# Performance work log

Measured on AMD Instinct MI355X. Metric: run time of the kernel, lower is better.

Reference implementation:

```python
import math
import jax, jax.numpy as jnp
import numpy as np

N_NODES = 50000
N_EDGES = 600000
IN_CH = 64      # in_channels == out_channels (residual requires it)
HEADS = 2
C = 64          # per-head dim == out_channels
HC = HEADS * C  # 128
EDGE_DIM = 32


def setup_inputs() -> dict:
    key = jax.random.key(0)
    ks = jax.random.split(key, 12)
    s = 0.05
    return {
        "x": jax.random.normal(ks[0], (N_NODES, IN_CH), jnp.float32),
        "edge_index": jax.random.randint(ks[1], (2, N_EDGES), 0, N_NODES, dtype=jnp.int64),
        "edge_attr": jax.random.normal(ks[2], (N_EDGES, EDGE_DIM), jnp.float32),
        "Wq": s * jax.random.normal(ks[3], (IN_CH, HC), jnp.float32),
        "bq": jnp.zeros((HC,), jnp.float32),
        "Wk": s * jax.random.normal(ks[4], (IN_CH, HC), jnp.float32),
        "bk": jnp.zeros((HC,), jnp.float32),
        "Wv": s * jax.random.normal(ks[5], (IN_CH, HC), jnp.float32),
        "bv": jnp.zeros((HC,), jnp.float32),
        "We": s * jax.random.normal(ks[6], (EDGE_DIM, HC), jnp.float32),
        "Wp": s * jax.random.normal(ks[7], (HC, IN_CH), jnp.float32),
        "bp": jnp.zeros((IN_CH,), jnp.float32),
        "ln1_g": jnp.ones((IN_CH,), jnp.float32),
        "ln1_b": jnp.zeros((IN_CH,), jnp.float32),
        "ln2_g": jnp.ones((IN_CH,), jnp.float32),
        "ln2_b": jnp.zeros((IN_CH,), jnp.float32),
        "W1": s * jax.random.normal(ks[8], (IN_CH, IN_CH), jnp.float32),
        "b1": jnp.zeros((IN_CH,), jnp.float32),
        "W2": s * jax.random.normal(ks[9], (IN_CH, IN_CH), jnp.float32),
        "b2": jnp.zeros((IN_CH,), jnp.float32),
    }


def _layernorm(x, g, b, eps=1e-5):
    m = jnp.mean(x, axis=-1, keepdims=True)
    v = jnp.mean(jnp.square(x - m), axis=-1, keepdims=True)
    return (x - m) / jnp.sqrt(v + eps) * g + b


def reference(x, edge_index, edge_attr, Wq, bq, Wk, bk, Wv, bv, We, Wp, bp,
              ln1_g, ln1_b, ln2_g, ln2_b, W1, b1, W2, b2):
    n = x.shape[0]
    residual = x
    h = _layernorm(x, ln1_g, ln1_b)
    q = (h @ Wq + bq).reshape(n, HEADS, C)
    k = (h @ Wk + bk).reshape(n, HEADS, C)
    v = (h @ Wv + bv).reshape(n, HEADS, C)

    src, tgt = edge_index[0], edge_index[1]
    e = (edge_attr @ We).reshape(-1, HEADS, C)   # (E,H,C)
    qi = q[tgt]                                  # (E,H,C) gather by target
    kj = k[src] + e
    vj = v[src] + e

    alpha = jnp.sum(qi * kj, axis=-1) / math.sqrt(C)            # (E,H)
    amax = jax.ops.segment_max(alpha, tgt, num_segments=n)      # (N,H)
    ex = jnp.exp(alpha - amax[tgt])
    den = jax.ops.segment_sum(ex, tgt, num_segments=n)          # (N,H)
    a = ex / (den[tgt] + 1e-8)                                  # (E,H)

    agg = jax.ops.segment_sum(a[:, :, None] * vj, tgt, num_segments=n)  # (N,H,C)
    out = agg.reshape(n, HC) @ Wp + bp
    out = out + residual                        # in_channels == out_channels

    res2 = out
    o = _layernorm(out, ln2_g, ln2_b)
    o = jax.nn.gelu(o @ W1 + b1, approximate=False) @ W2 + b2
    return o + res2
```

## Files before the change

### kernel.cpp

```cpp
#include <hip/hip_runtime.h>
#include <math.h>
#include <stdint.h>


typedef float f32x4 __attribute__((ext_vector_type(4)));
typedef __bf16 bf16x8 __attribute__((ext_vector_type(8)));
typedef unsigned int u32x4 __attribute__((ext_vector_type(4)));

#define WPM_S 200
#define W1_OFF 12800
#define W2_OFF 18432
#define W_TOT 24064
#define H_S 72
#define WC_S 72
#define WC_TOT (448 * 72)

__device__ __forceinline__ unsigned pack_bf16(float2 v) {
    unsigned a = __builtin_bit_cast(unsigned, v.x);
    unsigned b = __builtin_bit_cast(unsigned, v.y);
    a = (a + 0x7FFFu + ((a >> 16) & 1u)) >> 16;
    b = (b + 0x7FFFu + ((b >> 16) & 1u)) >> 16;
    return a | (b << 16);
}
__device__ __forceinline__ float2 unpack_bf16(unsigned p) {
    float x = __builtin_bit_cast(float, p << 16);
    float y = __builtin_bit_cast(float, p & 0xFFFF0000u);
    return make_float2(x, y);
}
__device__ __forceinline__ unsigned short bf16r(float x) {
    unsigned u = __builtin_bit_cast(unsigned, x);
    return (unsigned short)((u + 0x7FFFu + ((u >> 16) & 1u)) >> 16);
}

__device__ __forceinline__ f32x4 mfma16(bf16x8 a, bf16x8 b, f32x4 c) {
    return __builtin_amdgcn_mfma_f32_16x16x32_bf16(a, b, c, 0, 0, 0);
}
__device__ __forceinline__ bf16x8 frag_ld(const unsigned short* p) {
    return __builtin_bit_cast(bf16x8, *(const u32x4*)p);
}

__global__ void k_pre(const float* __restrict__ Wq, const float* __restrict__ Wk,
                      const float* __restrict__ Wv, const float* __restrict__ We,
                      const float* __restrict__ Wp, const float* __restrict__ W1,
                      const float* __restrict__ W2, const float* __restrict__ bq,
                      const float* __restrict__ bk, const float* __restrict__ bv,
                      unsigned short* __restrict__ wsW,
                      unsigned short* __restrict__ wcat, float* __restrict__ bcat,
                      int* __restrict__ deg, int n) {
    int idx = blockIdx.x * 256 + threadIdx.x;
    for (int i = idx; i < n; i += gridDim.x * 256) deg[i] = 0;
    if (idx < 8192) {
        int o = idx >> 7, k = idx & 127;
        wsW[o * WPM_S + k] = bf16r(Wp[((k & 1) * 64 + (k >> 1)) * 64 + o]);
        int cin = idx >> 7, j = idx & 127;
        wcat[j * WC_S + cin] = bf16r(Wq[cin * 128 + j]);
        wcat[(128 + j) * WC_S + cin] = bf16r(Wk[cin * 128 + j]);
        wcat[(256 + j) * WC_S + cin] = bf16r(Wv[cin * 128 + j]);
    }
    if (idx < 4096) {
        int o = idx >> 6, k = idx & 63;
        wsW[W1_OFF + o * 88 + k] = bf16r(W1[k * 64 + o]);
        wsW[W2_OFF + o * 88 + k] = bf16r(W2[k * 64 + o]);
        int o2 = idx & 63, dh = idx >> 6, d = dh >> 1, h = dh & 1;
        float s = 0.f;
        for (int c = 0; c < 64; ++c)
            s += We[d * 128 + h * 64 + c] * Wp[(h * 64 + c) * 64 + o2];
        wsW[o2 * WPM_S + 128 + dh] = bf16r(s);
        int cin2 = idx & 63, dh2 = idx >> 6, d2 = dh2 >> 1, h2 = dh2 & 1;
        float s2 = 0.f;
        for (int c = 0; c < 64; ++c)
            s2 += Wq[cin2 * 128 + h2 * 64 + c] * We[d2 * 128 + h2 * 64 + c];
        wcat[(384 + dh2) * WC_S + cin2] = bf16r(s2);
    }
    if (idx < 384)
        bcat[idx] = idx < 128 ? bq[idx] : idx < 256 ? bk[idx - 128] : bv[idx - 256];
    if (idx < 64) {
        int d = idx >> 1, h = idx & 1;
        float s = 0.f;
        for (int c = 0; c < 64; ++c)
            s += bq[h * 64 + c] * We[d * 128 + h * 64 + c];
        bcat[384 + idx] = s;
    }
}

__global__ __launch_bounds__(256) void k_bucket(
    const int* __restrict__ ei, int* __restrict__ deg,
    int* __restrict__ bucket_e, unsigned short* __restrict__ bucket_s,
    int E, int n) {
    int e = blockIdx.x * 256 + threadIdx.x;
    if (e >= E) return;
    int src = ei[e], tgt = ei[E + e];
    src = min(max(src, 0), n - 1);
    tgt = min(max(tgt, 0), n - 1);
    int slot = atomicAdd(&deg[tgt], 1);
    if (slot < 64) {
        bucket_e[(size_t)tgt * 64 + slot] = e;
        bucket_s[(size_t)tgt * 64 + slot] = (unsigned short)src;
    }
}

__global__ __launch_bounds__(256) void k_qkv(
    const float* __restrict__ x, const unsigned short* __restrict__ wcat,
    const float* __restrict__ bcat,
    const float* __restrict__ g1, const float* __restrict__ b1,
    unsigned* __restrict__ qx, unsigned* __restrict__ kbf,
    unsigned* __restrict__ vbf, int n) {
    __shared__ __align__(16) unsigned short sW[WC_TOT];
    int tid = threadIdx.x;
    for (int i = tid; i < WC_TOT / 8; i += 256)
        ((u32x4*)sW)[i] = ((const u32x4*)wcat)[i];
    __syncthreads();

    int wave = tid >> 6, lane = tid & 63;
    int cl = lane & 15, kg = lane >> 4;
    int node0 = blockIdx.x * 64 + wave * 16;
    if (node0 >= n) return;
    int arow = min(node0 + cl, n - 1);

    const float4* xp = (const float4*)(x + (size_t)arow * 64);
    float4 xv[4] = {xp[kg * 2], xp[kg * 2 + 1], xp[8 + kg * 2], xp[9 + kg * 2]};
    float s1 = 0.f, s2 = 0.f;
#pragma unroll
    for (int i = 0; i < 4; ++i) {
        s1 += (xv[i].x + xv[i].y) + (xv[i].z + xv[i].w);
        s2 += xv[i].x * xv[i].x + xv[i].y * xv[i].y
            + xv[i].z * xv[i].z + xv[i].w * xv[i].w;
    }
    s1 += __shfl_xor(s1, 16); s2 += __shfl_xor(s2, 16);
    s1 += __shfl_xor(s1, 32); s2 += __shfl_xor(s2, 32);
    float mean = s1 * 0.015625f;
    float var  = s2 * 0.015625f - mean * mean;
    float rstd = rsqrtf(var + 1e-5f);
    const float4* gp = (const float4*)g1;
    const float4* bp1 = (const float4*)b1;
    float4 gv[4] = {gp[kg * 2], gp[kg * 2 + 1], gp[8 + kg * 2], gp[9 + kg * 2]};
    float4 bv4[4] = {bp1[kg * 2], bp1[kg * 2 + 1], bp1[8 + kg * 2], bp1[9 + kg * 2]};
    unsigned fr[8];
#pragma unroll
    for (int i = 0; i < 4; ++i) {
        float h0 = (xv[i].x - mean) * rstd * gv[i].x + bv4[i].x;
        float h1 = (xv[i].y - mean) * rstd * gv[i].y + bv4[i].y;
        float h2 = (xv[i].z - mean) * rstd * gv[i].z + bv4[i].z;
        float h3 = (xv[i].w - mean) * rstd * gv[i].w + bv4[i].w;
        fr[i * 2]     = pack_bf16(make_float2(h0, h1));
        fr[i * 2 + 1] = pack_bf16(make_float2(h2, h3));
    }
    bf16x8 A0 = __builtin_bit_cast(bf16x8, (u32x4){fr[0], fr[1], fr[2], fr[3]});
    bf16x8 A1 = __builtin_bit_cast(bf16x8, (u32x4){fr[4], fr[5], fr[6], fr[7]});

#pragma unroll
    for (int tq = 0; tq < 4; ++tq) {
        int c = tq * 16 + cl;
        f32x4 aq0 = {bcat[c], bcat[c], bcat[c], bcat[c]};
        float b_;
        b_ = bcat[64 + c];  f32x4 aq1 = {b_, b_, b_, b_};
        b_ = bcat[128 + c]; f32x4 ak0 = {b_, b_, b_, b_};
        b_ = bcat[192 + c]; f32x4 ak1 = {b_, b_, b_, b_};
        b_ = bcat[256 + c]; f32x4 av0 = {b_, b_, b_, b_};
        b_ = bcat[320 + c]; f32x4 av1 = {b_, b_, b_, b_};
        b_ = bcat[384 + c]; f32x4 aw  = {b_, b_, b_, b_};
#pragma unroll
        for (int s = 0; s < 2; ++s) {
            bf16x8 A = s ? A1 : A0;
            int ko = s * 32 + kg * 8;
            aq0 = mfma16(A, frag_ld(sW + (size_t)(c) * WC_S + ko), aq0);
            aq1 = mfma16(A, frag_ld(sW + (size_t)(64 + c) * WC_S + ko), aq1);
            ak0 = mfma16(A, frag_ld(sW + (size_t)(128 + c) * WC_S + ko), ak0);
            ak1 = mfma16(A, frag_ld(sW + (size_t)(192 + c) * WC_S + ko), ak1);
            av0 = mfma16(A, frag_ld(sW + (size_t)(256 + c) * WC_S + ko), av0);
            av1 = mfma16(A, frag_ld(sW + (size_t)(320 + c) * WC_S + ko), av1);
            aw  = mfma16(A, frag_ld(sW + (size_t)(384 + c) * WC_S + ko), aw);
        }
#pragma unroll
        for (int j = 0; j < 4; ++j) {
            int node = node0 + kg * 4 + j;
            if (node < n) {
                qx[(size_t)node * 128 + c] = pack_bf16(make_float2(aq0[j], aq1[j]));
                kbf[(size_t)node * 64 + c] = pack_bf16(make_float2(ak0[j], ak1[j]));
                vbf[(size_t)node * 64 + c] = pack_bf16(make_float2(av0[j], av1[j]));
                ((float*)qx)[(size_t)node * 128 + 64 + c] = aw[j];
            }
        }
    }
}

__global__ __launch_bounds__(256) void k_attn(
    const unsigned* __restrict__ qx, const unsigned* __restrict__ kbf,
    const unsigned* __restrict__ vbf, const float* __restrict__ edge_attr,
    const int* __restrict__ deg, const int* __restrict__ bucket_e,
    const unsigned short* __restrict__ bucket_s,
    unsigned* __restrict__ aggs, int n, int E) {
    int wave = threadIdx.x >> 6, lane = threadIdx.x & 63;
    int node = blockIdx.x * 4 + wave;
    if (node >= n) return;
    int sub = lane >> 4, l = lane & 15;

    uint4 qq = ((const uint4*)qx)[(size_t)node * 32 + l];
    float4 w4 = ((const float4*)qx)[(size_t)node * 32 + 16 + l];
    float2 q0 = unpack_bf16(qq.x), q1 = unpack_bf16(qq.y),
           q2 = unpack_bf16(qq.z), q3 = unpack_bf16(qq.w);

    int dcount = min(deg[node], 64);
    int eid_l = 0, src_l = 0;
    if (lane < dcount) {
        eid_l = min(max(bucket_e[(size_t)node * 64 + lane], 0), E - 1);
        src_l = min((int)bucket_s[(size_t)node * 64 + lane], n - 1);
    }

    const uint4* kb4 = (const uint4*)kbf;
    const uint4* vb4 = (const uint4*)vbf;
    const float2* ea2 = (const float2*)edge_attr;

    float accA[4] = {0.f, 0.f, 0.f, 0.f}, accB[4] = {0.f, 0.f, 0.f, 0.f};
    float aS0 = 0.f, aS1 = 0.f, bS0 = 0.f, bS1 = 0.f;
    float den0 = 0.f, den1 = 0.f;

    uint4 kk, vv; float2 a2;
    {
        int jj = sub & 63;
        int ej = __shfl(eid_l, jj), sj = __shfl(src_l, jj);
        kk = kb4[(size_t)sj * 16 + l];
        vv = vb4[(size_t)sj * 16 + l];
        a2 = ea2[(size_t)ej * 16 + l];
    }
    for (int i = 0; i < dcount; i += 4) {
        uint4 kc = kk, vc = vv; float2 ac = a2;
        bool valid = (i + sub) < dcount;
        int inx = i + 4;
        if (inx < dcount) {
            int jj = (inx + sub) & 63;
            int ej = __shfl(eid_l, jj), sj = __shfl(src_l, jj);
            kk = kb4[(size_t)sj * 16 + l];
            vv = vb4[(size_t)sj * 16 + l];
            a2 = ea2[(size_t)ej * 16 + l];
        }
        float2 k0 = unpack_bf16(kc.x), k1 = unpack_bf16(kc.y),
               k2 = unpack_bf16(kc.z), k3 = unpack_bf16(kc.w);
        float r0 = q0.x * k0.x + q1.x * k1.x + q2.x * k2.x + q3.x * k3.x
                 + w4.x * ac.x + w4.z * ac.y;
        float r1 = q0.y * k0.y + q1.y * k1.y + q2.y * k2.y + q3.y * k3.y
                 + w4.y * ac.x + w4.w * ac.y;
#pragma unroll
        for (int m = 1; m < 16; m <<= 1) {
            r0 += __shfl_xor(r0, m);
            r1 += __shfl_xor(r1, m);
        }
        float ex0 = valid ? __expf(r0 * 0.125f) : 0.f;
        float ex1 = valid ? __expf(r1 * 0.125f) : 0.f;
        float2 v0 = unpack_bf16(vc.x), v1 = unpack_bf16(vc.y),
               v2 = unpack_bf16(vc.z), v3 = unpack_bf16(vc.w);
        accA[0] += ex0 * v0.x; accB[0] += ex1 * v0.y;
        accA[1] += ex0 * v1.x; accB[1] += ex1 * v1.y;
        accA[2] += ex0 * v2.x; accB[2] += ex1 * v2.y;
        accA[3] += ex0 * v3.x; accB[3] += ex1 * v3.y;
        aS0 += ex0 * ac.x; aS1 += ex1 * ac.x;
        bS0 += ex0 * ac.y; bS1 += ex1 * ac.y;
        den0 += ex0; den1 += ex1;
    }

#pragma unroll
    for (int m = 16; m < 64; m <<= 1) {
#pragma unroll
        for (int j = 0; j < 4; ++j) {
            accA[j] += __shfl_xor(accA[j], m);
            accB[j] += __shfl_xor(accB[j], m);
        }
        aS0 += __shfl_xor(aS0, m); aS1 += __shfl_xor(aS1, m);
        bS0 += __shfl_xor(bS0, m); bS1 += __shfl_xor(bS1, m);
        den0 += __shfl_xor(den0, m); den1 += __shfl_xor(den1, m);
    }

    float r0 = 1.0f / (den0 + 1e-8f);
    float r1 = 1.0f / (den1 + 1e-8f);

    float va = sub == 0 ? accA[0] : sub == 1 ? accA[1] : sub == 2 ? accA[2] : accA[3];
    float vb = sub == 0 ? accB[0] : sub == 1 ? accB[1] : sub == 2 ? accB[2] : accB[3];
    aggs[(size_t)node * 96 + 4 * l + sub] =
        pack_bf16(make_float2(va * r0, vb * r1));

    if (sub == 0) {
        unsigned s0 = pack_bf16(make_float2(aS0 * r0, aS1 * r1));
        unsigned s1 = pack_bf16(make_float2(bS0 * r0, bS1 * r1));
        *(uint2*)&aggs[(size_t)node * 96 + 64 + 2 * l] = make_uint2(s0, s1);
    }
}

__global__ __launch_bounds__(256) void k_post(
    const unsigned short* __restrict__ aggsb,
    const unsigned short* __restrict__ wsW,
    const float* __restrict__ bp, const float* __restrict__ x,
    const float* __restrict__ g2, const float* __restrict__ b2,
    const float* __restrict__ b1f, const float* __restrict__ b2f,
    float* __restrict__ out, int n) {
    __shared__ __align__(16) unsigned short sW[W_TOT];
    __shared__ __align__(16) unsigned short hb[4][2][16 * H_S];
    int tid = threadIdx.x;
    for (int i = tid; i < W_TOT / 8; i += 256)
        ((u32x4*)sW)[i] = ((const u32x4*)wsW)[i];
    __syncthreads();

    int wave = tid >> 6, lane = tid & 63;
    int cl = lane & 15, kg = lane >> 4;
    unsigned short* h2 = hb[wave][0];
    unsigned short* h3 = hb[wave][1];

    float bp_c[4], g2_c[4], b2_c[4], b1_c[4], bf2_c[4];
#pragma unroll
    for (int t = 0; t < 4; ++t) {
        int c = t * 16 + cl;
        bp_c[t] = bp[c];
        g2_c[t] = g2[c];
        b2_c[t] = b2[c];
        b1_c[t] = b1f[c];
        bf2_c[t] = b2f[c];
    }

    int wid = blockIdx.x * 4 + wave;
    int nbatch = (n + 15) >> 4;
    int nwaves = gridDim.x * 4;
    for (int bt = wid; bt < nbatch; bt += nwaves) {
        int node0 = bt * 16;

        f32x4 acc1[4];
#pragma unroll
        for (int t = 0; t < 4; ++t) acc1[t] = (f32x4){0.f, 0.f, 0.f, 0.f};
        int arow = min(node0 + cl, n - 1);
#pragma unroll
        for (int s = 0; s < 6; ++s) {
            bf16x8 af = frag_ld(aggsb + (size_t)arow * 192 + s * 32 + kg * 8);
#pragma unroll
            for (int t = 0; t < 4; ++t) {
                bf16x8 bf = frag_ld(sW + (t * 16 + cl) * WPM_S + s * 32 + kg * 8);
                acc1[t] = mfma16(af, bf, acc1[t]);
            }
        }
#pragma unroll
        for (int t = 0; t < 4; ++t) {
#pragma unroll
            for (int j = 0; j < 4; ++j) {
                int nd = min(node0 + kg * 4 + j, n - 1);
                acc1[t][j] += bp_c[t] + x[(size_t)nd * 64 + t * 16 + cl];
            }
        }

        float mean[4], rstd[4];
#pragma unroll
        for (int j = 0; j < 4; ++j) {
            float s1 = acc1[0][j] + acc1[1][j] + acc1[2][j] + acc1[3][j];
            float s2 = acc1[0][j] * acc1[0][j] + acc1[1][j] * acc1[1][j]
                     + acc1[2][j] * acc1[2][j] + acc1[3][j] * acc1[3][j];
#pragma unroll
            for (int m = 1; m < 16; m <<= 1) {
                s1 += __shfl_xor(s1, m);
                s2 += __shfl_xor(s2, m);
            }
            mean[j] = s1 * 0.015625f;
            float var = s2 * 0.015625f - mean[j] * mean[j];
            rstd[j] = rsqrtf(var + 1e-5f);
        }
#pragma unroll
        for (int t = 0; t < 4; ++t)
#pragma unroll
            for (int j = 0; j < 4; ++j) {
                float v = (acc1[t][j] - mean[j]) * rstd[j] * g2_c[t] + b2_c[t];
                h2[(kg * 4 + j) * H_S + t * 16 + cl] = bf16r(v);
            }
        asm volatile("s_waitcnt lgkmcnt(0)" ::: "memory");

        f32x4 acc2[4];
#pragma unroll
        for (int t = 0; t < 4; ++t)
            acc2[t] = (f32x4){b1_c[t], b1_c[t], b1_c[t], b1_c[t]};
#pragma unroll
        for (int s = 0; s < 2; ++s) {
            bf16x8 af = frag_ld(h2 + cl * H_S + s * 32 + kg * 8);
#pragma unroll
            for (int t = 0; t < 4; ++t) {
                bf16x8 bf = frag_ld(sW + W1_OFF + (t * 16 + cl) * 88 + s * 32 + kg * 8);
                acc2[t] = mfma16(af, bf, acc2[t]);
            }
        }
#pragma unroll
        for (int t = 0; t < 4; ++t)
#pragma unroll
            for (int j = 0; j < 4; ++j) {
                float v = acc2[t][j];
                v = 0.5f * v * (1.0f + erff(v * 0.70710678118654752f));
                h3[(kg * 4 + j) * H_S + t * 16 + cl] = bf16r(v);
            }
        asm volatile("s_waitcnt lgkmcnt(0)" ::: "memory");

        f32x4 acc3[4];
#pragma unroll
        for (int t = 0; t < 4; ++t) {
            acc3[t] = acc1[t];
#pragma unroll
            for (int j = 0; j < 4; ++j) acc3[t][j] += bf2_c[t];
        }
#pragma unroll
        for (int s = 0; s < 2; ++s) {
            bf16x8 af = frag_ld(h3 + cl * H_S + s * 32 + kg * 8);
#pragma unroll
            for (int t = 0; t < 4; ++t) {
                bf16x8 bf = frag_ld(sW + W2_OFF + (t * 16 + cl) * 88 + s * 32 + kg * 8);
                acc3[t] = mfma16(af, bf, acc3[t]);
            }
        }
#pragma unroll
        for (int t = 0; t < 4; ++t)
#pragma unroll
            for (int j = 0; j < 4; ++j) {
                int r = node0 + kg * 4 + j;
                if (r < n) out[(size_t)r * 64 + t * 16 + cl] = acc3[t][j];
            }
    }
}

extern "C" void kernel_launch(void* const* d_in, const int* in_sizes, int n_in,
                              void* d_out, int out_size, void* d_ws, size_t ws_size,
                              hipStream_t stream) {
    const float* x  = (const float*)d_in[0];
    const int*   ei = (const int*)d_in[1];
    const float* ea = (const float*)d_in[2];
    const float* Wq = (const float*)d_in[3];
    const float* bq = (const float*)d_in[4];
    const float* Wk = (const float*)d_in[5];
    const float* bk = (const float*)d_in[6];
    const float* Wv = (const float*)d_in[7];
    const float* bv = (const float*)d_in[8];
    const float* We = (const float*)d_in[9];
    const float* Wp = (const float*)d_in[10];
    const float* bp = (const float*)d_in[11];
    const float* g1 = (const float*)d_in[12];
    const float* b1 = (const float*)d_in[13];
    const float* g2 = (const float*)d_in[14];
    const float* b2 = (const float*)d_in[15];
    const float* W1 = (const float*)d_in[16];
    const float* b1f = (const float*)d_in[17];
    const float* W2 = (const float*)d_in[18];
    const float* b2f = (const float*)d_in[19];

    const int n = in_sizes[0] / 64;
    const int E = in_sizes[2] / 32;

    char* p = (char*)d_ws;
    unsigned* qx = (unsigned*)p; p += (size_t)n * 128 * 4;
    unsigned* kbf = (unsigned*)p; p += (size_t)n * 64 * 4;
    unsigned* vbf = (unsigned*)p; p += (size_t)n * 64 * 4;
    int* deg   = (int*)p;   p += (size_t)n * 4;
    p = (char*)(((uintptr_t)p + 15) & ~(uintptr_t)15);
    int* bucket_e = (int*)p; p += (size_t)n * 64 * 4;
    unsigned short* bucket_s = (unsigned short*)p; p += (size_t)n * 64 * 2;
    p = (char*)(((uintptr_t)p + 15) & ~(uintptr_t)15);
    unsigned* aggs = (unsigned*)p; p += (size_t)n * 96 * 4;
    unsigned short* wsW = (unsigned short*)p; p += W_TOT * 2;
    unsigned short* wcat = (unsigned short*)p; p += (size_t)WC_TOT * 2;
    float* bcat = (float*)p; p += 448 * 4;

    k_pre<<<196, 256, 0, stream>>>(Wq, Wk, Wv, We, Wp, W1, W2, bq, bk, bv,
                                   wsW, wcat, bcat, deg, n);
    k_bucket<<<(E + 255) / 256, 256, 0, stream>>>(ei, deg, bucket_e, bucket_s,
                                                  E, n);
    k_qkv<<<(n + 63) / 64, 256, 0, stream>>>(x, wcat, bcat, g1, b1,
                                             qx, kbf, vbf, n);
    k_attn<<<(n + 3) / 4, 256, 0, stream>>>(qx, kbf, vbf, ea, deg,
                                            bucket_e, bucket_s, aggs, n, E);
    int nb16 = (n + 15) >> 4;
    int blocks = (nb16 + 3) / 4;
    if (blocks > 391) blocks = 391;
    k_post<<<blocks, 256, 0, stream>>>((const unsigned short*)aggs, wsW,
                                       bp, x, g2, b2, b1f, b2f,
                                       (float*)d_out, n);
}
```

Before: 293.4 us.

## Use persistent grid-stride attention waves with two-deep gather prefetch and prescaled q

```diff
diff --git a/kernel.cpp b/kernel.cpp
--- a/kernel.cpp
+++ b/kernel.cpp
@@ -175,10 +175,11 @@
         for (int j = 0; j < 4; ++j) {
             int node = node0 + kg * 4 + j;
             if (node < n) {
-                qx[(size_t)node * 128 + c] = pack_bf16(make_float2(aq0[j], aq1[j]));
+                qx[(size_t)node * 128 + c] =
+                    pack_bf16(make_float2(aq0[j] * 0.125f, aq1[j] * 0.125f));
                 kbf[(size_t)node * 64 + c] = pack_bf16(make_float2(ak0[j], ak1[j]));
                 vbf[(size_t)node * 64 + c] = pack_bf16(make_float2(av0[j], av1[j]));
-                ((float*)qx)[(size_t)node * 128 + 64 + c] = aw[j];
+                ((float*)qx)[(size_t)node * 128 + 64 + c] = aw[j] * 0.125f;
             }
         }
     }
@@ -191,97 +192,108 @@
     const unsigned short* __restrict__ bucket_s,
     unsigned* __restrict__ aggs, int n, int E) {
     int wave = threadIdx.x >> 6, lane = threadIdx.x & 63;
-    int node = blockIdx.x * 4 + wave;
-    if (node >= n) return;
     int sub = lane >> 4, l = lane & 15;
-
-    uint4 qq = ((const uint4*)qx)[(size_t)node * 32 + l];
-    float4 w4 = ((const float4*)qx)[(size_t)node * 32 + 16 + l];
-    float2 q0 = unpack_bf16(qq.x), q1 = unpack_bf16(qq.y),
-           q2 = unpack_bf16(qq.z), q3 = unpack_bf16(qq.w);
-
-    int dcount = min(deg[node], 64);
-    int eid_l = 0, src_l = 0;
-    if (lane < dcount) {
-        eid_l = min(max(bucket_e[(size_t)node * 64 + lane], 0), E - 1);
-        src_l = min((int)bucket_s[(size_t)node * 64 + lane], n - 1);
-    }
-
+    int wid = blockIdx.x * 4 + wave;
+    int nw = gridDim.x * 4;
     const uint4* kb4 = (const uint4*)kbf;
     const uint4* vb4 = (const uint4*)vbf;
     const float2* ea2 = (const float2*)edge_attr;
 
-    float accA[4] = {0.f, 0.f, 0.f, 0.f}, accB[4] = {0.f, 0.f, 0.f, 0.f};
-    float aS0 = 0.f, aS1 = 0.f, bS0 = 0.f, bS1 = 0.f;
-    float den0 = 0.f, den1 = 0.f;
-
-    uint4 kk, vv; float2 a2;
-    {
-        int jj = sub & 63;
-        int ej = __shfl(eid_l, jj), sj = __shfl(src_l, jj);
-        kk = kb4[(size_t)sj * 16 + l];
-        vv = vb4[(size_t)sj * 16 + l];
-        a2 = ea2[(size_t)ej * 16 + l];
-    }
-    for (int i = 0; i < dcount; i += 4) {
-        uint4 kc = kk, vc = vv; float2 ac = a2;
-        bool valid = (i + sub) < dcount;
-        int inx = i + 4;
-        if (inx < dcount) {
-            int jj = (inx + sub) & 63;
+    for (int node = wid; node < n; node += nw) {
+        uint4 qq = ((const uint4*)qx)[(size_t)node * 32 + l];
+        float4 w4 = ((const float4*)qx)[(size_t)node * 32 + 16 + l];
+        float2 q0 = unpack_bf16(qq.x), q1 = unpack_bf16(qq.y),
+               q2 = unpack_bf16(qq.z), q3 = unpack_bf16(qq.w);
+
+        int dcount = min(deg[node], 64);
+        int eid_l = 0, src_l = 0;
+        if (lane < dcount) {
+            eid_l = min(max(bucket_e[(size_t)node * 64 + lane], 0), E - 1);
+            src_l = min((int)bucket_s[(size_t)node * 64 + lane], n - 1);
+        }
+
+        float accA[4] = {0.f, 0.f, 0.f, 0.f}, accB[4] = {0.f, 0.f, 0.f, 0.f};
+        float aS0 = 0.f, aS1 = 0.f, bS0 = 0.f, bS1 = 0.f;
+        float den0 = 0.f, den1 = 0.f;
+
+        uint4 kkA, vvA, kkB, vvB; float2 aA, aB;
+        {
+            int jj = sub;
             int ej = __shfl(eid_l, jj), sj = __shfl(src_l, jj);
-            kk = kb4[(size_t)sj * 16 + l];
-            vv = vb4[(size_t)sj * 16 + l];
-            a2 = ea2[(size_t)ej * 16 + l];
-        }
-        float2 k0 = unpack_bf16(kc.x), k1 = unpack_bf16(kc.y),
-               k2 = unpack_bf16(kc.z), k3 = unpack_bf16(kc.w);
-        float r0 = q0.x * k0.x + q1.x * k1.x + q2.x * k2.x + q3.x * k3.x
-                 + w4.x * ac.x + w4.z * ac.y;
-        float r1 = q0.y * k0.y + q1.y * k1.y + q2.y * k2.y + q3.y * k3.y
-                 + w4.y * ac.x + w4.w * ac.y;
-#pragma unroll
-        for (int m = 1; m < 16; m <<= 1) {
-            r0 += __shfl_xor(r0, m);
-            r1 += __shfl_xor(r1, m);
-        }
-        float ex0 = valid ? __expf(r0 * 0.125f) : 0.f;
-        float ex1 = valid ? __expf(r1 * 0.125f) : 0.f;
-        float2 v0 = unpack_bf16(vc.x), v1 = unpack_bf16(vc.y),
-               v2 = unpack_bf16(vc.z), v3 = unpack_bf16(vc.w);
-        accA[0] += ex0 * v0.x; accB[0] += ex1 * v0.y;
-        accA[1] += ex0 * v1.x; accB[1] += ex1 * v1.y;
-        accA[2] += ex0 * v2.x; accB[2] += ex1 * v2.y;
-        accA[3] += ex0 * v3.x; accB[3] += ex1 * v3.y;
-        aS0 += ex0 * ac.x; aS1 += ex1 * ac.x;
-        bS0 += ex0 * ac.y; bS1 += ex1 * ac.y;
-        den0 += ex0; den1 += ex1;
-    }
-
-#pragma unroll
-    for (int m = 16; m < 64; m <<= 1) {
-#pragma unroll
-        for (int j = 0; j < 4; ++j) {
-            accA[j] += __shfl_xor(accA[j], m);
-            accB[j] += __shfl_xor(accB[j], m);
-        }
-        aS0 += __shfl_xor(aS0, m); aS1 += __shfl_xor(aS1, m);
-        bS0 += __shfl_xor(bS0, m); bS1 += __shfl_xor(bS1, m);
-        den0 += __shfl_xor(den0, m); den1 += __shfl_xor(den1, m);
-    }
-
-    float r0 = 1.0f / (den0 + 1e-8f);
-    float r1 = 1.0f / (den1 + 1e-8f);
-
-    float va = sub == 0 ? accA[0] : sub == 1 ? accA[1] : sub == 2 ? accA[2] : accA[3];
-    float vb = sub == 0 ? accB[0] : sub == 1 ? accB[1] : sub == 2 ? accB[2] : accB[3];
-    aggs[(size_t)node * 96 + 4 * l + sub] =
-        pack_bf16(make_float2(va * r0, vb * r1));
-
-    if (sub == 0) {
-        unsigned s0 = pack_bf16(make_float2(aS0 * r0, aS1 * r1));
-        unsigned s1 = pack_bf16(make_float2(bS0 * r0, bS1 * r1));
-        *(uint2*)&aggs[(size_t)node * 96 + 64 + 2 * l] = make_uint2(s0, s1);
+            kkA = kb4[(size_t)sj * 16 + l];
+            vvA = vb4[(size_t)sj * 16 + l];
+            aA  = ea2[(size_t)ej * 16 + l];
+        }
+        {
+            int jj = (4 + sub) & 63;
+            int ej = __shfl(eid_l, jj), sj = __shfl(src_l, jj);
+            kkB = kb4[(size_t)sj * 16 + l];
+            vvB = vb4[(size_t)sj * 16 + l];
+            aB  = ea2[(size_t)ej * 16 + l];
+        }
+        for (int i = 0; i < dcount; i += 4) {
+            uint4 kc = kkA, vc = vvA; float2 ac = aA;
+            kkA = kkB; vvA = vvB; aA = aB;
+            bool valid = (i + sub) < dcount;
+            int inx = i + 8;
+            if (inx < dcount) {
+                int jj = (inx + sub) & 63;
+                int ej = __shfl(eid_l, jj), sj = __shfl(src_l, jj);
+                kkB = kb4[(size_t)sj * 16 + l];
+                vvB = vb4[(size_t)sj * 16 + l];
+                aB  = ea2[(size_t)ej * 16 + l];
+            }
+            float2 k0 = unpack_bf16(kc.x), k1 = unpack_bf16(kc.y),
+                   k2 = unpack_bf16(kc.z), k3 = unpack_bf16(kc.w);
+            float r0 = q0.x * k0.x + q1.x * k1.x + q2.x * k2.x + q3.x * k3.x
+                     + w4.x * ac.x + w4.z * ac.y;
+            float r1 = q0.y * k0.y + q1.y * k1.y + q2.y * k2.y + q3.y * k3.y
+                     + w4.y * ac.x + w4.w * ac.y;
+#pragma unroll
+            for (int m = 1; m < 16; m <<= 1) {
+                r0 += __shfl_xor(r0, m);
+                r1 += __shfl_xor(r1, m);
+            }
+            float ex0 = valid ? __expf(r0) : 0.f;
+            float ex1 = valid ? __expf(r1) : 0.f;
+            float2 v0 = unpack_bf16(vc.x), v1 = unpack_bf16(vc.y),
+                   v2 = unpack_bf16(vc.z), v3 = unpack_bf16(vc.w);
+            accA[0] += ex0 * v0.x; accB[0] += ex1 * v0.y;
+            accA[1] += ex0 * v1.x; accB[1] += ex1 * v1.y;
+            accA[2] += ex0 * v2.x; accB[2] += ex1 * v2.y;
+            accA[3] += ex0 * v3.x; accB[3] += ex1 * v3.y;
+            aS0 += ex0 * ac.x; aS1 += ex1 * ac.x;
+            bS0 += ex0 * ac.y; bS1 += ex1 * ac.y;
+            den0 += ex0; den1 += ex1;
+        }
+
+#pragma unroll
+        for (int m = 16; m < 64; m <<= 1) {
+#pragma unroll
+            for (int j = 0; j < 4; ++j) {
+                accA[j] += __shfl_xor(accA[j], m);
+                accB[j] += __shfl_xor(accB[j], m);
+            }
+            aS0 += __shfl_xor(aS0, m); aS1 += __shfl_xor(aS1, m);
+            bS0 += __shfl_xor(bS0, m); bS1 += __shfl_xor(bS1, m);
+            den0 += __shfl_xor(den0, m); den1 += __shfl_xor(den1, m);
+        }
+
+        float r0 = 1.0f / (den0 + 1e-8f);
+        float r1 = 1.0f / (den1 + 1e-8f);
+
+        float va = sub == 0 ? accA[0] : sub == 1 ? accA[1]
+                 : sub == 2 ? accA[2] : accA[3];
+        float vb = sub == 0 ? accB[0] : sub == 1 ? accB[1]
+                 : sub == 2 ? accB[2] : accB[3];
+        aggs[(size_t)node * 96 + 4 * l + sub] =
+            pack_bf16(make_float2(va * r0, vb * r1));
+
+        if (sub == 0) {
+            unsigned s0 = pack_bf16(make_float2(aS0 * r0, aS1 * r1));
+            unsigned s1 = pack_bf16(make_float2(bS0 * r0, bS1 * r1));
+            *(uint2*)&aggs[(size_t)node * 96 + 64 + 2 * l] = make_uint2(s0, s1);
+        }
     }
 }
 
@@ -463,8 +475,8 @@
                                                   E, n);
     k_qkv<<<(n + 63) / 64, 256, 0, stream>>>(x, wcat, bcat, g1, b1,
                                              qx, kbf, vbf, n);
-    k_attn<<<(n + 3) / 4, 256, 0, stream>>>(qx, kbf, vbf, ea, deg,
-                                            bucket_e, bucket_s, aggs, n, E);
+    k_attn<<<2048, 256, 0, stream>>>(qx, kbf, vbf, ea, deg,
+                                     bucket_e, bucket_s, aggs, n, E);
     int nb16 = (n + 15) >> 4;
     int blocks = (nb16 + 3) / 4;
     if (blocks > 391) blocks = 391;
```

New measurement: 308.6 us. 1.05x slower.
